# Kernel tuning notes

Measured on AMD Instinct MI355X. Metric: run time of the kernel, lower is better.

Reference implementation:

```python
import jax, jax.numpy as jnp
import numpy as np

NA_CUTOFF = 30.0
OTHER_CUTOFF = 15.0
THRESHOLDS = jnp.array([0.5, 1.0, 2.0, 4.0], dtype=jnp.float32)


def _cdist(x):
    # x: [b, n, 3] -> [b, n, n] euclidean distances, safe-sqrt (0 grad at 0)
    diff = x[:, :, None, :] - x[:, None, :, :]
    sq = jnp.sum(diff * diff, axis=-1)
    safe = jnp.where(sq > 0, sq, 1.0)
    return jnp.where(sq > 0, jnp.sqrt(safe), 0.0)


def setup_inputs() -> dict:
    key = jax.random.key(0)
    k1, k2, k3, k4, k5 = jax.random.split(key, 5)
    b, n = 2, 4096
    # angstrom-scale coordinates so cutoffs (15/30 A) are meaningful
    true_coords = jax.random.normal(k1, (b, n, 3), dtype=jnp.float32) * 20.0
    pred_coords = true_coords + jax.random.normal(k2, (b, n, 3), dtype=jnp.float32) * 1.0
    is_dna = jax.random.randint(k3, (b, n), 0, 2) > 0
    is_rna = jax.random.randint(k4, (b, n), 0, 2) > 0
    coords_mask = jax.random.randint(k5, (b, n), 0, 2) > 0
    return {
        'pred_coords': pred_coords,
        'true_coords': true_coords,
        'is_dna': is_dna,
        'is_rna': is_rna,
        'coords_mask': coords_mask,
    }


def reference(pred_coords, true_coords, is_dna, is_rna, coords_mask):
    b, n, _ = pred_coords.shape
    pred_dists = _cdist(pred_coords)            # [b, n, n]
    true_dists = _cdist(true_coords)            # [b, n, n]
    dist_diff = jnp.abs(true_dists - pred_dists)
    # eps: sigmoid(threshold - |d_true - d_pred|), averaged over 4 thresholds
    eps = jax.nn.sigmoid(THRESHOLDS - dist_diff[..., None]).mean(axis=-1)  # [b, n, n]

    is_nt = is_dna | is_rna
    nt_pair = is_nt[:, :, None] & is_nt[:, None, :]
    inclusion = jnp.where(nt_pair, true_dists < NA_CUTOFF, true_dists < OTHER_CUTOFF)
    mask = inclusion & ~jnp.eye(n, dtype=bool)[None]
    mask = mask & (coords_mask[:, :, None] & coords_mask[:, None, :])

    maskf = mask.astype(eps.dtype)
    num = (eps * maskf).sum(axis=(-1, -2))
    den = jnp.maximum(maskf.sum(axis=(-1, -2)), 1.0)
    lddt = num / den
    return 1.0 - lddt.mean()
```

## Files before the change

kernel.cpp:

```cpp
#include <hip/hip_runtime.h>
#include <math.h>

#define NTHREADS 256
#define CAP 4096
#define NSBLK 544

#define LUTN 3072
#define OCT_LO (-16)
#define U_MIN 1.52587890625e-5f
#define U_MAX 255.999f
#define IDX_BYTE_BIAS 56832u

typedef float v2f __attribute__((ext_vector_type(2)));

__device__ __forceinline__ float fsqrt(float x) {
#if __has_builtin(__builtin_amdgcn_sqrtf)
    return __builtin_amdgcn_sqrtf(x);
#else
    return sqrtf(x);
#endif
}
__device__ __forceinline__ float fmed3(float x, float lo, float hi) {
#if __has_builtin(__builtin_amdgcn_fmed3f)
    return __builtin_amdgcn_fmed3f(x, lo, hi);
#else
    return fminf(fmaxf(x, lo), hi);
#endif
}

__device__ __forceinline__ float sig4(float d) {
    const float e = expf(d);
    return 1.0f / (1.0f + e * 0.60653065971263342360f)
         + 1.0f / (1.0f + e * 0.36787944117144232160f)
         + 1.0f / (1.0f + e * 0.13533528323661269189f)
         + 1.0f / (1.0f + e * 0.01831563888873418029f);
}

__global__ __launch_bounds__(256) void prep_kernel(
    float* __restrict__ gLUT, float* __restrict__ C, int* __restrict__ Mcnt, int S)
{
    const int gid = blockIdx.x * 256 + threadIdx.x;
    if (gid < LUTN) {
        const int oct = gid >> 7;
        const int k   = gid & 127;
        const float base2 = exp2f((float)(oct + OCT_LO));
        const float umid = base2 * (1.0f + ((float)k + 0.5f) * 0.0078125f);
        gLUT[gid] = sig4(fsqrt(umid));
    }
    if (gid < 2) Mcnt[gid] = 0;
    const int total = 9 * S;
    const int stride = gridDim.x * 256;
    for (int idx = gid; idx < total; idx += stride)
        C[idx] = (idx < 6 * S) ? 1.0e9f : 0.0f;
}

__global__ __launch_bounds__(256) void compact_kernel(
    const float* __restrict__ pred, const float* __restrict__ tru,
    const int* __restrict__ dna, const int* __restrict__ rna,
    const int* __restrict__ cm,
    float* __restrict__ C, int* __restrict__ Mcnt, int n, int S)
{
    __shared__ int scan[256];
    __shared__ int sbase;
    const int chunks = n / 256;
    const int b = blockIdx.x / chunks;
    const int chunk = blockIdx.x % chunks;
    const int tid = threadIdx.x;
    const size_t gi = (size_t)b * n + chunk * 256 + tid;

    const int f = (cm[gi] != 0) ? 1 : 0;
    scan[tid] = f;
    __syncthreads();
    #pragma unroll
    for (int off = 1; off < 256; off <<= 1) {
        const int v = scan[tid];
        const int u = (tid >= off) ? scan[tid - off] : 0;
        __syncthreads();
        scan[tid] = v + u;
        __syncthreads();
    }
    if (tid == 255) sbase = atomicAdd(&Mcnt[b], scan[255]);
    __syncthreads();

    if (f) {
        const int pos = sbase + scan[tid] - 1;
        const float* p = pred + gi * 3;
        const float* q = tru  + gi * 3;
        const int nt = (dna[gi] != 0) || (rna[gi] != 0);
        const int bo = b * CAP;
        C[0 * S + bo + pos] = p[0];  C[1 * S + bo + pos] = p[1];
        C[2 * S + bo + pos] = p[2];  C[3 * S + bo + pos] = q[0];
        C[4 * S + bo + pos] = q[1];  C[5 * S + bo + pos] = q[2];
        C[6 * S + bo + pos] = nt ? 900.0f : 225.0f;
        C[7 * S + bo + pos] = 225.0f;
        C[8 * S + bo + pos] = nt ? 1.0f : 0.0f;
    }
}

__device__ __forceinline__ void pair_tail(float sqp, float sqt, float cut2,
                                          const char* __restrict__ lutB,
                                          float& num, float& den) {
    const float r  = fsqrt(sqt * sqp);
    const float u0 = fmaf(-2.0f, r, sqt + sqp);
    const float u  = fmed3(u0, U_MIN, U_MAX);
    const unsigned int bits = __float_as_uint(u);
    const float s  = *(const float*)(lutB + ((bits >> 14) & ~3u));
    const float m  = (sqt < cut2) ? 1.0f : 0.0f;
    num = fmaf(m, s, num);
    den += m;
}

__global__ __launch_bounds__(NTHREADS) void lddt_tile_kernel(
    const float* __restrict__ C, const int* __restrict__ Mptr,
    const float* __restrict__ gLUT,
    float* __restrict__ pnum, float* __restrict__ pden, int S)
{
    __shared__ __align__(16) float sPX[256], sPY[256], sPZ[256];
    __shared__ __align__(16) float sTX[256], sTY[256], sTZ[256];
    __shared__ __align__(16) float sCut[2 * 256];
    __shared__ __align__(16) float sLUT[LUTN];
    __shared__ float wnum[4], wden[4];

    const int tid = threadIdx.x;

    int s = blockIdx.x;
    const int bi = s / NSBLK;
    s -= bi * NSBLK;
    const int q = s >> 2;
    const int r = s & 3;
    const int W = 33;
    int g = (int)(((float)W - fsqrt((float)(W * W - 8 * q))) * 0.5f);
    while ((g + 1) * 16 - ((g + 1) * g) / 2 <= q) ++g;
    while (g * 16 - (g * (g - 1)) / 2 > q) --g;
    const int sc = g + (q - (g * 16 - (g * (g - 1)) / 2));
    const int ti = 4 * g + r;
    const int i0 = 64 * ti;
    const int J0 = 256 * sc;
    const bool has_diag = (sc == g);
    const int M = Mptr[bi];

    if (i0 >= M || J0 >= M) {
        if (tid == 0) { pnum[blockIdx.x] = 0.0f; pden[blockIdx.x] = 0.0f; }
        return;
    }

    const int bo = bi * CAP;
    const float* cpx = C + 0 * S + bo;  const float* cpy = C + 1 * S + bo;
    const float* cpz = C + 2 * S + bo;  const float* ctx = C + 3 * S + bo;
    const float* cty = C + 4 * S + bo;  const float* ctz = C + 5 * S + bo;
    const float* ccn = C + 6 * S + bo;  const float* cco = C + 7 * S + bo;
    const float* cntf = C + 8 * S + bo;

    {
        const float4* gl4 = (const float4*)gLUT;
        float4* sl4 = (float4*)sLUT;
        #pragma unroll
        for (int e = tid; e < LUTN / 4; e += NTHREADS) sl4[e] = gl4[e];
    }
    {
        const int j = J0 + tid;
        sPX[tid] = cpx[j]; sPY[tid] = cpy[j]; sPZ[tid] = cpz[j];
        sTX[tid] = ctx[j]; sTY[tid] = cty[j]; sTZ[tid] = ctz[j];
        sCut[tid] = ccn[j]; sCut[256 + tid] = cco[j];
    }

    const int w = tid >> 6;
    const int l = tid & 63;
    const int i = i0 + l;
    const float pix = cpx[i], piy = cpy[i], piz = cpz[i];
    const float tix = ctx[i], tiy = cty[i], tiz = ctz[i];
    const bool nti = (cntf[i] != 0.0f);
    __syncthreads();

    const float* cutsel = nti ? &sCut[0] : &sCut[256];
    const char* lutB = (const char*)sLUT - IDX_BYTE_BIAS;
    const int kbase = 16 * w;

    const v2f px2 = {pix, pix}, py2 = {piy, piy}, pz2 = {piz, piz};
    const v2f tx2 = {tix, tix}, ty2 = {tiy, tiy}, tz2 = {tiz, tiz};

    float accn = 0.0f, accd = 0.0f;

    #pragma unroll
    for (int c = 0; c < 4; ++c) {
        const int tj = 4 * sc + c;
        if (tj < ti || 64 * tj >= M) continue;
        const bool diag = has_diag && (c == r);
        const int o = 64 * c;

        float num = 0.0f, den = 0.0f;
        #pragma unroll
        for (int qd = 0; qd < 4; ++qd) {
            const int jq = o + kbase + 4 * qd;
            const float4 PX = *(const float4*)&sPX[jq];
            const float4 PY = *(const float4*)&sPY[jq];
            const float4 PZ = *(const float4*)&sPZ[jq];
            const float4 TX = *(const float4*)&sTX[jq];
            const float4 TY = *(const float4*)&sTY[jq];
            const float4 TZ = *(const float4*)&sTZ[jq];
            const float4 CTC = *(const float4*)&cutsel[jq];

            v2f dx, dy, dz, sqpA, sqpB, sqtA, sqtB;

            dx = px2 - (v2f){PX.x, PX.y}; dy = py2 - (v2f){PY.x, PY.y}; dz = pz2 - (v2f){PZ.x, PZ.y};
            sqpA = dx * dx + dy * dy + dz * dz;
            dx = tx2 - (v2f){TX.x, TX.y}; dy = ty2 - (v2f){TY.x, TY.y}; dz = tz2 - (v2f){TZ.x, TZ.y};
            sqtA = dx * dx + dy * dy + dz * dz;

            dx = px2 - (v2f){PX.z, PX.w}; dy = py2 - (v2f){PY.z, PY.w}; dz = pz2 - (v2f){PZ.z, PZ.w};
            sqpB = dx * dx + dy * dy + dz * dz;
            dx = tx2 - (v2f){TX.z, TX.w}; dy = ty2 - (v2f){TY.z, TY.w}; dz = tz2 - (v2f){TZ.z, TZ.w};
            sqtB = dx * dx + dy * dy + dz * dz;

            pair_tail(sqpA.x, sqtA.x, CTC.x, lutB, num, den);
            pair_tail(sqpA.y, sqtA.y, CTC.y, lutB, num, den);
            pair_tail(sqpB.x, sqtB.x, CTC.z, lutB, num, den);
            pair_tail(sqpB.y, sqtB.y, CTC.w, lutB, num, den);
        }
        const float sc2 = diag ? 1.0f : 2.0f;
        accn = fmaf(sc2, num, accn);
        accd = fmaf(sc2, den, accd);
    }

    if (has_diag && ((l >> 4) == w) && i < M) {
        accn -= sLUT[0];
        accd -= 1.0f;
    }

    #pragma unroll
    for (int off = 32; off > 0; off >>= 1) {
        accn += __shfl_down(accn, off, 64);
        accd += __shfl_down(accd, off, 64);
    }
    if ((tid & 63) == 0) { wnum[w] = accn; wden[w] = accd; }
    __syncthreads();

    if (tid == 0) {
        pnum[blockIdx.x] = wnum[0] + wnum[1] + wnum[2] + wnum[3];
        pden[blockIdx.x] = wden[0] + wden[1] + wden[2] + wden[3];
    }
}

__global__ __launch_bounds__(256) void lddt_final_kernel(
    const float* __restrict__ pnum, const float* __restrict__ pden,
    float* __restrict__ out, int nsblk)
{
    __shared__ double sn0[4], sn1[4], sd0[4], sd1[4];
    double n0 = 0, n1 = 0, d0 = 0, d1 = 0;
    for (int s = threadIdx.x; s < 2 * nsblk; s += 256) {
        if (s < nsblk) { n0 += (double)pnum[s]; d0 += (double)pden[s]; }
        else           { n1 += (double)pnum[s]; d1 += (double)pden[s]; }
    }
    #pragma unroll
    for (int off = 32; off > 0; off >>= 1) {
        n0 += __shfl_down(n0, off, 64); d0 += __shfl_down(d0, off, 64);
        n1 += __shfl_down(n1, off, 64); d1 += __shfl_down(d1, off, 64);
    }
    const int w = threadIdx.x >> 6;
    if ((threadIdx.x & 63) == 0) { sn0[w] = n0; sn1[w] = n1; sd0[w] = d0; sd1[w] = d1; }
    __syncthreads();
    if (threadIdx.x == 0) {
        double N0 = sn0[0] + sn0[1] + sn0[2] + sn0[3];
        double N1 = sn1[0] + sn1[1] + sn1[2] + sn1[3];
        double D0 = sd0[0] + sd0[1] + sd0[2] + sd0[3];
        double D1 = sd1[0] + sd1[1] + sd1[2] + sd1[3];
        D0 = D0 > 1.0 ? D0 : 1.0;
        D1 = D1 > 1.0 ? D1 : 1.0;
        const double l0 = 0.25 * N0 / D0;
        const double l1 = 0.25 * N1 / D1;
        out[0] = (float)(1.0 - 0.5 * (l0 + l1));
    }
}

extern "C" void kernel_launch(void* const* d_in, const int* in_sizes, int n_in,
                              void* d_out, int out_size, void* d_ws, size_t ws_size,
                              hipStream_t stream) {
    const float* pred = (const float*)d_in[0];
    const float* tru  = (const float*)d_in[1];
    const int*   dna  = (const int*)d_in[2];
    const int*   rna  = (const int*)d_in[3];
    const int*   cm   = (const int*)d_in[4];
    float* out = (float*)d_out;

    const int B = 2;
    const int n = in_sizes[2] / B;
    const int S = B * CAP;

    char* p = (char*)d_ws;
    float* gLUT = (float*)p;                 p += (size_t)LUTN * sizeof(float);
    float* C    = (float*)p;                 p += (size_t)9 * S * sizeof(float);
    float* pnum = (float*)p;                 p += (size_t)B * NSBLK * sizeof(float);
    float* pden = (float*)p;                 p += (size_t)B * NSBLK * sizeof(float);
    int*   Mcnt = (int*)p;

    hipLaunchKernelGGL(prep_kernel, dim3(288), dim3(256), 0, stream,
                       gLUT, C, Mcnt, S);
    hipLaunchKernelGGL(compact_kernel, dim3(B * (n / 256)), dim3(256), 0, stream,
                       pred, tru, dna, rna, cm, C, Mcnt, n, S);
    hipLaunchKernelGGL(lddt_tile_kernel, dim3(B * NSBLK), dim3(NTHREADS), 0, stream,
                       C, Mcnt, gLUT, pnum, pden, S);
    hipLaunchKernelGGL(lddt_final_kernel, dim3(1), dim3(256), 0, stream,
                       pnum, pden, out, NSBLK);
}
```

Before: 78.04 us.

## Fuse prep, compaction, tile and final reduction into one cooperative kernel

```diff
diff --git a/kernel.cpp b/kernel.cpp
--- a/kernel.cpp
+++ b/kernel.cpp
@@ -1,9 +1,14 @@
 #include <hip/hip_runtime.h>
+#include <hip/hip_cooperative_groups.h>
 #include <math.h>
+
+namespace cg = cooperative_groups;
 
 #define NTHREADS 256
 #define CAP 4096
 #define NSBLK 544
+#define NBATCH 2
+#define NTILES (NBATCH * NSBLK)
 
 #define LUTN 3072
 #define OCT_LO (-16)
@@ -34,67 +39,6 @@
          + 1.0f / (1.0f + e * 0.36787944117144232160f)
          + 1.0f / (1.0f + e * 0.13533528323661269189f)
          + 1.0f / (1.0f + e * 0.01831563888873418029f);
-}
-
-__global__ __launch_bounds__(256) void prep_kernel(
-    float* __restrict__ gLUT, float* __restrict__ C, int* __restrict__ Mcnt, int S)
-{
-    const int gid = blockIdx.x * 256 + threadIdx.x;
-    if (gid < LUTN) {
-        const int oct = gid >> 7;
-        const int k   = gid & 127;
-        const float base2 = exp2f((float)(oct + OCT_LO));
-        const float umid = base2 * (1.0f + ((float)k + 0.5f) * 0.0078125f);
-        gLUT[gid] = sig4(fsqrt(umid));
-    }
-    if (gid < 2) Mcnt[gid] = 0;
-    const int total = 9 * S;
-    const int stride = gridDim.x * 256;
-    for (int idx = gid; idx < total; idx += stride)
-        C[idx] = (idx < 6 * S) ? 1.0e9f : 0.0f;
-}
-
-__global__ __launch_bounds__(256) void compact_kernel(
-    const float* __restrict__ pred, const float* __restrict__ tru,
-    const int* __restrict__ dna, const int* __restrict__ rna,
-    const int* __restrict__ cm,
-    float* __restrict__ C, int* __restrict__ Mcnt, int n, int S)
-{
-    __shared__ int scan[256];
-    __shared__ int sbase;
-    const int chunks = n / 256;
-    const int b = blockIdx.x / chunks;
-    const int chunk = blockIdx.x % chunks;
-    const int tid = threadIdx.x;
-    const size_t gi = (size_t)b * n + chunk * 256 + tid;
-
-    const int f = (cm[gi] != 0) ? 1 : 0;
-    scan[tid] = f;
-    __syncthreads();
-    #pragma unroll
-    for (int off = 1; off < 256; off <<= 1) {
-        const int v = scan[tid];
-        const int u = (tid >= off) ? scan[tid - off] : 0;
-        __syncthreads();
-        scan[tid] = v + u;
-        __syncthreads();
-    }
-    if (tid == 255) sbase = atomicAdd(&Mcnt[b], scan[255]);
-    __syncthreads();
-
-    if (f) {
-        const int pos = sbase + scan[tid] - 1;
-        const float* p = pred + gi * 3;
-        const float* q = tru  + gi * 3;
-        const int nt = (dna[gi] != 0) || (rna[gi] != 0);
-        const int bo = b * CAP;
-        C[0 * S + bo + pos] = p[0];  C[1 * S + bo + pos] = p[1];
-        C[2 * S + bo + pos] = p[2];  C[3 * S + bo + pos] = q[0];
-        C[4 * S + bo + pos] = q[1];  C[5 * S + bo + pos] = q[2];
-        C[6 * S + bo + pos] = nt ? 900.0f : 225.0f;
-        C[7 * S + bo + pos] = 225.0f;
-        C[8 * S + bo + pos] = nt ? 1.0f : 0.0f;
-    }
 }
 
 __device__ __forceinline__ void pair_tail(float sqp, float sqt, float cut2,
@@ -110,165 +54,231 @@
     den += m;
 }
 
-__global__ __launch_bounds__(NTHREADS) void lddt_tile_kernel(
-    const float* __restrict__ C, const int* __restrict__ Mptr,
-    const float* __restrict__ gLUT,
-    float* __restrict__ pnum, float* __restrict__ pden, int S)
+__global__ __launch_bounds__(NTHREADS) void fused_lddt_kernel(
+    const float* __restrict__ pred, const float* __restrict__ tru,
+    const int* __restrict__ dna, const int* __restrict__ rna,
+    const int* __restrict__ cm,
+    float* __restrict__ C, int* __restrict__ Mtot,
+    float* __restrict__ pnum, float* __restrict__ pden,
+    float* __restrict__ out, int n, int S)
 {
     __shared__ __align__(16) float sPX[256], sPY[256], sPZ[256];
     __shared__ __align__(16) float sTX[256], sTY[256], sTZ[256];
     __shared__ __align__(16) float sCut[2 * 256];
     __shared__ __align__(16) float sLUT[LUTN];
     __shared__ float wnum[4], wden[4];
+    __shared__ int scanArr[256];
+    __shared__ int wsum[4];
+    __shared__ double sn0[4], sn1[4], sd0[4], sd1[4];
 
     const int tid = threadIdx.x;
-
-    int s = blockIdx.x;
-    const int bi = s / NSBLK;
-    s -= bi * NSBLK;
-    const int q = s >> 2;
-    const int r = s & 3;
-    const int W = 33;
-    int g = (int)(((float)W - fsqrt((float)(W * W - 8 * q))) * 0.5f);
-    while ((g + 1) * 16 - ((g + 1) * g) / 2 <= q) ++g;
-    while (g * 16 - (g * (g - 1)) / 2 > q) --g;
-    const int sc = g + (q - (g * 16 - (g * (g - 1)) / 2));
-    const int ti = 4 * g + r;
-    const int i0 = 64 * ti;
-    const int J0 = 256 * sc;
-    const bool has_diag = (sc == g);
-    const int M = Mptr[bi];
-
-    if (i0 >= M || J0 >= M) {
-        if (tid == 0) { pnum[blockIdx.x] = 0.0f; pden[blockIdx.x] = 0.0f; }
-        return;
-    }
-
-    const int bo = bi * CAP;
-    const float* cpx = C + 0 * S + bo;  const float* cpy = C + 1 * S + bo;
-    const float* cpz = C + 2 * S + bo;  const float* ctx = C + 3 * S + bo;
-    const float* cty = C + 4 * S + bo;  const float* ctz = C + 5 * S + bo;
-    const float* ccn = C + 6 * S + bo;  const float* cco = C + 7 * S + bo;
-    const float* cntf = C + 8 * S + bo;
-
-    {
-        const float4* gl4 = (const float4*)gLUT;
-        float4* sl4 = (float4*)sLUT;
-        #pragma unroll
-        for (int e = tid; e < LUTN / 4; e += NTHREADS) sl4[e] = gl4[e];
-    }
-    {
-        const int j = J0 + tid;
-        sPX[tid] = cpx[j]; sPY[tid] = cpy[j]; sPZ[tid] = cpz[j];
-        sTX[tid] = ctx[j]; sTY[tid] = cty[j]; sTZ[tid] = ctz[j];
-        sCut[tid] = ccn[j]; sCut[256 + tid] = cco[j];
-    }
-
-    const int w = tid >> 6;
-    const int l = tid & 63;
-    const int i = i0 + l;
-    const float pix = cpx[i], piy = cpy[i], piz = cpz[i];
-    const float tix = ctx[i], tiy = cty[i], tiz = ctz[i];
-    const bool nti = (cntf[i] != 0.0f);
-    __syncthreads();
-
-    const float* cutsel = nti ? &sCut[0] : &sCut[256];
+    const int bid = blockIdx.x;
+    const int chunks = n / 256;
+    const int nCompact = NBATCH * chunks;
+
+    for (int x = bid * NTHREADS + tid; x < NTILES; x += gridDim.x * NTHREADS) {
+        pnum[x] = 0.0f; pden[x] = 0.0f;
+    }
+
+    if (bid < nCompact) {
+        const int b = bid / chunks;
+        const int chunk = bid - b * chunks;
+        const size_t gb = (size_t)b * n;
+        const int gi = chunk * 256 + tid;
+        const int f = (cm[gb + gi] != 0) ? 1 : 0;
+
+        int pre = 0;
+        for (int c = 0; c < chunk; ++c)
+            pre += (cm[gb + c * 256 + tid] != 0) ? 1 : 0;
+        int v = pre;
+        #pragma unroll
+        for (int off = 32; off > 0; off >>= 1) v += __shfl_down(v, off, 64);
+        if ((tid & 63) == 0) wsum[tid >> 6] = v;
+        scanArr[tid] = f;
+        __syncthreads();
+        const int base = wsum[0] + wsum[1] + wsum[2] + wsum[3];
+
+        #pragma unroll
+        for (int off = 1; off < 256; off <<= 1) {
+            const int a = scanArr[tid];
+            const int u = (tid >= off) ? scanArr[tid - off] : 0;
+            __syncthreads();
+            scanArr[tid] = a + u;
+            __syncthreads();
+        }
+        if (f) {
+            const int pos = base + scanArr[tid] - 1;
+            const size_t gidx = gb + gi;
+            const float* p = pred + gidx * 3;
+            const float* tc = tru + gidx * 3;
+            const int nt = (dna[gidx] != 0) || (rna[gidx] != 0);
+            const int bo = b * CAP;
+            C[0 * S + bo + pos] = p[0];  C[1 * S + bo + pos] = p[1];
+            C[2 * S + bo + pos] = p[2];  C[3 * S + bo + pos] = tc[0];
+            C[4 * S + bo + pos] = tc[1]; C[5 * S + bo + pos] = tc[2];
+            C[6 * S + bo + pos] = nt ? 900.0f : 225.0f;
+            C[7 * S + bo + pos] = 225.0f;
+            C[8 * S + bo + pos] = nt ? 1.0f : 0.0f;
+        }
+        if (chunk == chunks - 1 && tid == 255) Mtot[b] = base + scanArr[255];
+    }
+
+    for (int e = tid; e < LUTN; e += NTHREADS) {
+        const int oct = e >> 7;
+        const int k   = e & 127;
+        const float base2 = exp2f((float)(oct + OCT_LO));
+        const float umid = base2 * (1.0f + ((float)k + 0.5f) * 0.0078125f);
+        sLUT[e] = sig4(fsqrt(umid));
+    }
+
+    cg::this_grid().sync();
+
     const char* lutB = (const char*)sLUT - IDX_BYTE_BIAS;
-    const int kbase = 16 * w;
-
-    const v2f px2 = {pix, pix}, py2 = {piy, piy}, pz2 = {piz, piz};
-    const v2f tx2 = {tix, tix}, ty2 = {tiy, tiy}, tz2 = {tiz, tiz};
-
-    float accn = 0.0f, accd = 0.0f;
-
-    #pragma unroll
-    for (int c = 0; c < 4; ++c) {
-        const int tj = 4 * sc + c;
-        if (tj < ti || 64 * tj >= M) continue;
-        const bool diag = has_diag && (c == r);
-        const int o = 64 * c;
-
-        float num = 0.0f, den = 0.0f;
-        #pragma unroll
-        for (int qd = 0; qd < 4; ++qd) {
-            const int jq = o + kbase + 4 * qd;
-            const float4 PX = *(const float4*)&sPX[jq];
-            const float4 PY = *(const float4*)&sPY[jq];
-            const float4 PZ = *(const float4*)&sPZ[jq];
-            const float4 TX = *(const float4*)&sTX[jq];
-            const float4 TY = *(const float4*)&sTY[jq];
-            const float4 TZ = *(const float4*)&sTZ[jq];
-            const float4 CTC = *(const float4*)&cutsel[jq];
-
-            v2f dx, dy, dz, sqpA, sqpB, sqtA, sqtB;
-
-            dx = px2 - (v2f){PX.x, PX.y}; dy = py2 - (v2f){PY.x, PY.y}; dz = pz2 - (v2f){PZ.x, PZ.y};
-            sqpA = dx * dx + dy * dy + dz * dz;
-            dx = tx2 - (v2f){TX.x, TX.y}; dy = ty2 - (v2f){TY.x, TY.y}; dz = tz2 - (v2f){TZ.x, TZ.y};
-            sqtA = dx * dx + dy * dy + dz * dz;
-
-            dx = px2 - (v2f){PX.z, PX.w}; dy = py2 - (v2f){PY.z, PY.w}; dz = pz2 - (v2f){PZ.z, PZ.w};
-            sqpB = dx * dx + dy * dy + dz * dz;
-            dx = tx2 - (v2f){TX.z, TX.w}; dy = ty2 - (v2f){TY.z, TY.w}; dz = tz2 - (v2f){TZ.z, TZ.w};
-            sqtB = dx * dx + dy * dy + dz * dz;
-
-            pair_tail(sqpA.x, sqtA.x, CTC.x, lutB, num, den);
-            pair_tail(sqpA.y, sqtA.y, CTC.y, lutB, num, den);
-            pair_tail(sqpB.x, sqtB.x, CTC.z, lutB, num, den);
-            pair_tail(sqpB.y, sqtB.y, CTC.w, lutB, num, den);
-        }
-        const float sc2 = diag ? 1.0f : 2.0f;
-        accn = fmaf(sc2, num, accn);
-        accd = fmaf(sc2, den, accd);
-    }
-
-    if (has_diag && ((l >> 4) == w) && i < M) {
-        accn -= sLUT[0];
-        accd -= 1.0f;
-    }
-
-    #pragma unroll
-    for (int off = 32; off > 0; off >>= 1) {
-        accn += __shfl_down(accn, off, 64);
-        accd += __shfl_down(accd, off, 64);
-    }
-    if ((tid & 63) == 0) { wnum[w] = accn; wden[w] = accd; }
-    __syncthreads();
-
-    if (tid == 0) {
-        pnum[blockIdx.x] = wnum[0] + wnum[1] + wnum[2] + wnum[3];
-        pden[blockIdx.x] = wden[0] + wden[1] + wden[2] + wden[3];
-    }
-}
-
-__global__ __launch_bounds__(256) void lddt_final_kernel(
-    const float* __restrict__ pnum, const float* __restrict__ pden,
-    float* __restrict__ out, int nsblk)
-{
-    __shared__ double sn0[4], sn1[4], sd0[4], sd1[4];
-    double n0 = 0, n1 = 0, d0 = 0, d1 = 0;
-    for (int s = threadIdx.x; s < 2 * nsblk; s += 256) {
-        if (s < nsblk) { n0 += (double)pnum[s]; d0 += (double)pden[s]; }
-        else           { n1 += (double)pnum[s]; d1 += (double)pden[s]; }
-    }
-    #pragma unroll
-    for (int off = 32; off > 0; off >>= 1) {
-        n0 += __shfl_down(n0, off, 64); d0 += __shfl_down(d0, off, 64);
-        n1 += __shfl_down(n1, off, 64); d1 += __shfl_down(d1, off, 64);
-    }
-    const int w = threadIdx.x >> 6;
-    if ((threadIdx.x & 63) == 0) { sn0[w] = n0; sn1[w] = n1; sd0[w] = d0; sd1[w] = d1; }
-    __syncthreads();
-    if (threadIdx.x == 0) {
-        double N0 = sn0[0] + sn0[1] + sn0[2] + sn0[3];
-        double N1 = sn1[0] + sn1[1] + sn1[2] + sn1[3];
-        double D0 = sd0[0] + sd0[1] + sd0[2] + sd0[3];
-        double D1 = sd1[0] + sd1[1] + sd1[2] + sd1[3];
-        D0 = D0 > 1.0 ? D0 : 1.0;
-        D1 = D1 > 1.0 ? D1 : 1.0;
-        const double l0 = 0.25 * N0 / D0;
-        const double l1 = 0.25 * N1 / D1;
-        out[0] = (float)(1.0 - 0.5 * (l0 + l1));
+    for (int s0 = bid; s0 < NTILES; s0 += gridDim.x) {
+        int s = s0;
+        const int bi = s / NSBLK;
+        s -= bi * NSBLK;
+        const int q = s >> 2;
+        const int r = s & 3;
+        const int W = 33;
+        int g = (int)(((float)W - fsqrt((float)(W * W - 8 * q))) * 0.5f);
+        while ((g + 1) * 16 - ((g + 1) * g) / 2 <= q) ++g;
+        while (g * 16 - (g * (g - 1)) / 2 > q) --g;
+        const int sc = g + (q - (g * 16 - (g * (g - 1)) / 2));
+        const int ti = 4 * g + r;
+        const int i0 = 64 * ti;
+        const int J0 = 256 * sc;
+        const bool has_diag = (sc == g);
+        const int M = Mtot[bi];
+        if (i0 >= M || J0 >= M) continue;
+
+        const int bo = bi * CAP;
+        const float* cpx = C + 0 * S + bo;  const float* cpy = C + 1 * S + bo;
+        const float* cpz = C + 2 * S + bo;  const float* ctx = C + 3 * S + bo;
+        const float* cty = C + 4 * S + bo;  const float* ctz = C + 5 * S + bo;
+        const float* ccn = C + 6 * S + bo;  const float* cco = C + 7 * S + bo;
+        const float* cntf = C + 8 * S + bo;
+
+        {
+            const int j = J0 + tid;
+            const bool jv = j < M;
+            sPX[tid] = jv ? cpx[j] : 1.0e9f;
+            sPY[tid] = jv ? cpy[j] : 1.0e9f;
+            sPZ[tid] = jv ? cpz[j] : 1.0e9f;
+            sTX[tid] = jv ? ctx[j] : 1.0e9f;
+            sTY[tid] = jv ? cty[j] : 1.0e9f;
+            sTZ[tid] = jv ? ctz[j] : 1.0e9f;
+            sCut[tid]       = jv ? ccn[j] : 0.0f;
+            sCut[256 + tid] = jv ? cco[j] : 0.0f;
+        }
+
+        const int w = tid >> 6;
+        const int l = tid & 63;
+        const int i = i0 + l;
+        const bool iv = i < M;
+        const float pix = iv ? cpx[i] : 1.0e9f;
+        const float piy = iv ? cpy[i] : 1.0e9f;
+        const float piz = iv ? cpz[i] : 1.0e9f;
+        const float tix = iv ? ctx[i] : 1.0e9f;
+        const float tiy = iv ? cty[i] : 1.0e9f;
+        const float tiz = iv ? ctz[i] : 1.0e9f;
+        const bool nti = iv ? (cntf[i] != 0.0f) : false;
+        __syncthreads();
+
+        const float* cutsel = nti ? &sCut[0] : &sCut[256];
+        const int kbase = 16 * w;
+
+        const v2f px2 = {pix, pix}, py2 = {piy, piy}, pz2 = {piz, piz};
+        const v2f tx2 = {tix, tix}, ty2 = {tiy, tiy}, tz2 = {tiz, tiz};
+
+        float accn = 0.0f, accd = 0.0f;
+
+        #pragma unroll
+        for (int c = 0; c < 4; ++c) {
+            const int tj = 4 * sc + c;
+            if (tj < ti || 64 * tj >= M) continue;
+            const bool diag = has_diag && (c == r);
+            const int o = 64 * c;
+
+            float num = 0.0f, den = 0.0f;
+            #pragma unroll
+            for (int qd = 0; qd < 4; ++qd) {
+                const int jq = o + kbase + 4 * qd;
+                const float4 PX = *(const float4*)&sPX[jq];
+                const float4 PY = *(const float4*)&sPY[jq];
+                const float4 PZ = *(const float4*)&sPZ[jq];
+                const float4 TX = *(const float4*)&sTX[jq];
+                const float4 TY = *(const float4*)&sTY[jq];
+                const float4 TZ = *(const float4*)&sTZ[jq];
+                const float4 CTC = *(const float4*)&cutsel[jq];
+
+                v2f dx, dy, dz, sqpA, sqpB, sqtA, sqtB;
+
+                dx = px2 - (v2f){PX.x, PX.y}; dy = py2 - (v2f){PY.x, PY.y}; dz = pz2 - (v2f){PZ.x, PZ.y};
+                sqpA = dx * dx + dy * dy + dz * dz;
+                dx = tx2 - (v2f){TX.x, TX.y}; dy = ty2 - (v2f){TY.x, TY.y}; dz = tz2 - (v2f){TZ.x, TZ.y};
+                sqtA = dx * dx + dy * dy + dz * dz;
+
+                dx = px2 - (v2f){PX.z, PX.w}; dy = py2 - (v2f){PY.z, PY.w}; dz = pz2 - (v2f){PZ.z, PZ.w};
+                sqpB = dx * dx + dy * dy + dz * dz;
+                dx = tx2 - (v2f){TX.z, TX.w}; dy = ty2 - (v2f){TY.z, TY.w}; dz = tz2 - (v2f){TZ.z, TZ.w};
+                sqtB = dx * dx + dy * dy + dz * dz;
+
+                pair_tail(sqpA.x, sqtA.x, CTC.x, lutB, num, den);
+                pair_tail(sqpA.y, sqtA.y, CTC.y, lutB, num, den);
+                pair_tail(sqpB.x, sqtB.x, CTC.z, lutB, num, den);
+                pair_tail(sqpB.y, sqtB.y, CTC.w, lutB, num, den);
+            }
+            const float sc2 = diag ? 1.0f : 2.0f;
+            accn = fmaf(sc2, num, accn);
+            accd = fmaf(sc2, den, accd);
+        }
+
+        if (has_diag && ((l >> 4) == w) && iv) {
+            accn -= sLUT[0];
+            accd -= 1.0f;
+        }
+
+        #pragma unroll
+        for (int off = 32; off > 0; off >>= 1) {
+            accn += __shfl_down(accn, off, 64);
+            accd += __shfl_down(accd, off, 64);
+        }
+        if ((tid & 63) == 0) { wnum[w] = accn; wden[w] = accd; }
+        __syncthreads();
+        if (tid == 0) {
+            pnum[s0] = wnum[0] + wnum[1] + wnum[2] + wnum[3];
+            pden[s0] = wden[0] + wden[1] + wden[2] + wden[3];
+        }
+    }
+
+    cg::this_grid().sync();
+
+    if (bid == 0) {
+        double n0 = 0, n1 = 0, d0 = 0, d1 = 0;
+        for (int x = tid; x < NTILES; x += NTHREADS) {
+            if (x < NSBLK) { n0 += (double)pnum[x]; d0 += (double)pden[x]; }
+            else           { n1 += (double)pnum[x]; d1 += (double)pden[x]; }
+        }
+        #pragma unroll
+        for (int off = 32; off > 0; off >>= 1) {
+            n0 += __shfl_down(n0, off, 64); d0 += __shfl_down(d0, off, 64);
+            n1 += __shfl_down(n1, off, 64); d1 += __shfl_down(d1, off, 64);
+        }
+        const int w2 = tid >> 6;
+        if ((tid & 63) == 0) { sn0[w2] = n0; sn1[w2] = n1; sd0[w2] = d0; sd1[w2] = d1; }
+        __syncthreads();
+        if (tid == 0) {
+            double N0 = sn0[0] + sn0[1] + sn0[2] + sn0[3];
+            double N1 = sn1[0] + sn1[1] + sn1[2] + sn1[3];
+            double D0 = sd0[0] + sd0[1] + sd0[2] + sd0[3];
+            double D1 = sd1[0] + sd1[1] + sd1[2] + sd1[3];
+            D0 = D0 > 1.0 ? D0 : 1.0;
+            D1 = D1 > 1.0 ? D1 : 1.0;
+            const double l0 = 0.25 * N0 / D0;
+            const double l1 = 0.25 * N1 / D1;
+            out[0] = (float)(1.0 - 0.5 * (l0 + l1));
+        }
     }
 }
 
@@ -280,25 +290,38 @@
     const int*   dna  = (const int*)d_in[2];
     const int*   rna  = (const int*)d_in[3];
     const int*   cm   = (const int*)d_in[4];
-    float* out = (float*)d_out;
-
-    const int B = 2;
-    const int n = in_sizes[2] / B;
-    const int S = B * CAP;
+    float* outp = (float*)d_out;
+
+    const int B = NBATCH;
+    int n = in_sizes[2] / B;
+    int S = B * CAP;
 
     char* p = (char*)d_ws;
-    float* gLUT = (float*)p;                 p += (size_t)LUTN * sizeof(float);
-    float* C    = (float*)p;                 p += (size_t)9 * S * sizeof(float);
-    float* pnum = (float*)p;                 p += (size_t)B * NSBLK * sizeof(float);
-    float* pden = (float*)p;                 p += (size_t)B * NSBLK * sizeof(float);
-    int*   Mcnt = (int*)p;
-
-    hipLaunchKernelGGL(prep_kernel, dim3(288), dim3(256), 0, stream,
-                       gLUT, C, Mcnt, S);
-    hipLaunchKernelGGL(compact_kernel, dim3(B * (n / 256)), dim3(256), 0, stream,
-                       pred, tru, dna, rna, cm, C, Mcnt, n, S);
-    hipLaunchKernelGGL(lddt_tile_kernel, dim3(B * NSBLK), dim3(NTHREADS), 0, stream,
-                       C, Mcnt, gLUT, pnum, pden, S);
-    hipLaunchKernelGGL(lddt_final_kernel, dim3(1), dim3(256), 0, stream,
-                       pnum, pden, out, NSBLK);
-}
+    float* C    = (float*)p;              p += (size_t)9 * S * sizeof(float);
+    float* pnum = (float*)p;              p += (size_t)NTILES * sizeof(float);
+    float* pden = (float*)p;              p += (size_t)NTILES * sizeof(float);
+    int*   Mtot = (int*)p;
+
+    static int s_gridCap = 0;
+    if (s_gridCap == 0) {
+        int nb = 0;
+        if (hipOccupancyMaxActiveBlocksPerMultiprocessor(&nb, fused_lddt_kernel,
+                                                         NTHREADS, 0) != hipSuccess || nb < 1)
+            nb = 1;
+        int dev = 0;
+        (void)hipGetDevice(&dev);
+        int cus = 0;
+        if (hipDeviceGetAttribute(&cus, hipDeviceAttributeMultiprocessorCount,
+                                  dev) != hipSuccess || cus <= 0)
+            cus = 256;
+        s_gridCap = nb * cus;
+    }
+    int gridBlocks = s_gridCap < NTILES ? s_gridCap : NTILES;
+    const int nCompact = B * (n / 256);
+    if (gridBlocks < nCompact) gridBlocks = nCompact;
+
+    void* args[] = { &pred, &tru, &dna, &rna, &cm,
+                     &C, &Mtot, &pnum, &pden, &outp, &n, &S };
+    hipLaunchCooperativeKernel(fused_lddt_kernel, dim3(gridBlocks),
+                               dim3(NTHREADS), args, 0, stream);
+}
```

New measurement: 135.8 us. 74.0% more time.
